# Kernel optimization log

Measured on AMD Instinct MI355X. Metric: run time of the kernel, lower is better.

## Reference

```python
import jax, jax.numpy as jnp
import numpy as np

RING_WORLD_SIZE = 4  # number of ring steps / KV sequence chunks


def _ring_flash_attention(q, k, v, ring_size):
    # q,k,v: [B, S, H, D]; non-causal full attention computed blockwise over
    # KV chunks (one per ring step) with numerically-stable online LSE merge,
    # mirroring _compact_ring_fwd + update_out_and_lse.
    B, S, H, D = q.shape
    scale = D ** (-0.5)
    chunk = S // ring_size
    out = None  # [B, S, H, D] accumulated in fp32
    lse = None  # [B, H, S] running log-sum-exp
    for step in range(ring_size):
        k_blk = jax.lax.dynamic_slice_in_dim(k, step * chunk, chunk, axis=1)
        v_blk = jax.lax.dynamic_slice_in_dim(v, step * chunk, chunk, axis=1)
        # scores: [B, H, Sq, Sk_blk]
        scores = jnp.einsum('bqhd,bkhd->bhqk', q, k_blk) * scale
        block_lse = jax.scipy.special.logsumexp(scores, axis=-1)  # [B,H,Sq]
        probs = jnp.exp(scores - block_lse[..., None])
        block_out = jnp.einsum('bhqk,bkhd->bqhd', probs, v_blk)
        if out is None:
            out, lse = block_out, block_lse
        else:
            new_lse = jnp.logaddexp(lse, block_lse)
            w_old = jnp.exp(lse - new_lse)       # [B,H,Sq]
            w_new = jnp.exp(block_lse - new_lse)
            # broadcast weights to [B,Sq,H,1]
            out = (jnp.transpose(w_old, (0, 2, 1))[..., None] * out
                   + jnp.transpose(w_new, (0, 2, 1))[..., None] * block_out)
            lse = new_lse
    return out.astype(q.dtype)


def setup_inputs() -> dict:
    key = jax.random.key(0)
    kq, kk, kv = jax.random.split(key, 3)
    shape = (1, 4096, 16, 128)
    return {
        'query': jax.random.normal(kq, shape, dtype=jnp.float32),
        'key': jax.random.normal(kk, shape, dtype=jnp.float32),
        'value': jax.random.normal(kv, shape, dtype=jnp.float32),
    }


def reference(query, key, value):
    # Ulysses all-to-all is identity on a single logical device; the ring loop
    # with lossless (error-feedback) KV compression reduces to blockwise
    # attention with online softmax merging.
    return _ring_flash_attention(query, key, value, RING_WORLD_SIZE)
```

## Files before the change

kernel.cpp:

```cpp
#include <hip/hip_runtime.h>
#include <hip/hip_bf16.h>

#define S_LEN 4096
#define NH    16
#define DD    128
#define HD    2048
#define QB    64
#define KB    64
#define NT    (S_LEN/KB)

typedef __bf16 bf16_t;
typedef bf16_t bf16x8 __attribute__((ext_vector_type(8)));
typedef float  f32x4  __attribute__((ext_vector_type(4)));

static __device__ __forceinline__ bf16x8 pack8(float4 a, float4 b, float s) {
  bf16x8 v;
  v[0]=(bf16_t)(a.x*s); v[1]=(bf16_t)(a.y*s); v[2]=(bf16_t)(a.z*s); v[3]=(bf16_t)(a.w*s);
  v[4]=(bf16_t)(b.x*s); v[5]=(bf16_t)(b.y*s); v[6]=(bf16_t)(b.z*s); v[7]=(bf16_t)(b.w*s);
  return v;
}

__global__ __launch_bounds__(256) void prep_k(const float* __restrict__ Kg,
                                              bf16_t* __restrict__ Kp) {
  const int kt = blockIdx.x, h = blockIdx.y, tid = threadIdx.x;
  __shared__ bf16_t tile[KB][DD + 8];
  #pragma unroll
  for (int it = 0; it < 8; ++it) {
    int lin4 = it*256 + tid;
    int r  = lin4 >> 5;
    int dc = (lin4 & 31) * 4;
    float4 a = *(const float4*)(Kg + (size_t)(kt*KB + r)*HD + h*DD + dc);
    tile[r][dc+0]=(bf16_t)a.x; tile[r][dc+1]=(bf16_t)a.y;
    tile[r][dc+2]=(bf16_t)a.z; tile[r][dc+3]=(bf16_t)a.w;
  }
  __syncthreads();
  bf16_t* out = Kp + (size_t)(h*NT + kt)*8192;
  #pragma unroll
  for (int it = 0; it < 4; ++it) {
    int cid = it*256 + tid;
    int f = cid >> 6, l = cid & 63;
    int b = f >> 2, c = f & 3;
    int row = b*16 + (l & 15);
    int d0  = c*32 + (l >> 4)*8;
    bf16x8 v = *(const bf16x8*)(&tile[row][d0]);
    *(bf16x8*)(out + (size_t)cid*8) = v;
  }
}

__global__ __launch_bounds__(256) void prep_v(const float* __restrict__ Vg,
                                              bf16_t* __restrict__ Vp) {
  const int kt = blockIdx.x, h = blockIdx.y, tid = threadIdx.x;
  __shared__ bf16_t tile[KB][DD + 8];
  #pragma unroll
  for (int it = 0; it < 8; ++it) {
    int lin4 = it*256 + tid;
    int r  = lin4 >> 5;
    int dc = (lin4 & 31) * 4;
    float4 a = *(const float4*)(Vg + (size_t)(kt*KB + r)*HD + h*DD + dc);
    tile[r][dc+0]=(bf16_t)a.x; tile[r][dc+1]=(bf16_t)a.y;
    tile[r][dc+2]=(bf16_t)a.z; tile[r][dc+3]=(bf16_t)a.w;
  }
  __syncthreads();
  bf16_t* out = Vp + (size_t)(h*NT + kt)*8192;
  #pragma unroll
  for (int it = 0; it < 4; ++it) {
    int cid = it*256 + tid;
    int f = cid >> 6, l = cid & 63;
    int ks = f >> 3, db = f & 7;
    int d  = db*16 + (l & 15);
    int c0 = ks*32 + (l >> 4)*8;
    bf16x8 v;
    #pragma unroll
    for (int m = 0; m < 8; ++m) {
      int c = c0 + m;
      int k = 32*(c>>5) + 16*((c>>2)&1) + 4*((c>>3)&3) + (c&3);
      v[m] = tile[k][d];
    }
    *(bf16x8*)(out + (size_t)cid*8) = v;
  }
}

__global__ __launch_bounds__(128, 2) void attn_fwd(const float* __restrict__ Qg,
                                                   const bf16_t* __restrict__ Kp,
                                                   const bf16_t* __restrict__ Vp,
                                                   float* __restrict__ Og) {
  const int phys = blockIdx.x;
  const int logical = (phys & 7) * 128 + (phys >> 3);
  const int h  = logical >> 6;
  const int qt = logical & 63;
  const int tid  = threadIdx.x;
  const int wid  = tid >> 6;
  const int lane = tid & 63;
  const int l16  = lane & 15;
  const int lg   = lane >> 4;
  const int lo16 = lane * 16;

  const float qs = 0.08838834764831845f * 1.4426950408889634f;
  bf16x8 qf[2][4];
  #pragma unroll
  for (int g = 0; g < 2; ++g) {
    const int qrow = qt*QB + wid*32 + g*16 + l16;
    const float* qp = Qg + (size_t)qrow*HD + h*DD + lg*8;
    #pragma unroll
    for (int c = 0; c < 4; ++c) {
      float4 a = *(const float4*)(qp + c*32);
      float4 b = *(const float4*)(qp + c*32 + 4);
      qf[g][c] = pack8(a, b, qs);
    }
  }
  bf16x8 onesf;
  #pragma unroll
  for (int j = 0; j < 8; ++j) onesf[j] = (bf16_t)1.0f;

  const char* KpH = (const char*)(Kp + (size_t)h*NT*8192) + lo16;
  const char* VpH = (const char*)(Vp + (size_t)h*NT*8192) + lo16;

  bf16x8 kreg[16];
  #pragma unroll
  for (int f = 0; f < 16; ++f) kreg[f] = *(const bf16x8*)(KpH + (f << 10));

  f32x4 acc[2][8];
  f32x4 acc_l[2];
  #pragma unroll
  for (int g = 0; g < 2; ++g) {
    #pragma unroll
    for (int i = 0; i < 8; ++i) acc[g][i] = (f32x4){0.f,0.f,0.f,0.f};
    acc_l[g] = (f32x4){0.f,0.f,0.f,0.f};
  }
  float m_run[2] = {-__builtin_inff(), -__builtin_inff()};

  for (int kt = 0; kt < NT; ++kt) {
    f32x4 sc[2][4];
    #pragma unroll
    for (int g = 0; g < 2; ++g)
      #pragma unroll
      for (int b = 0; b < 4; ++b) sc[g][b] = (f32x4){0.f,0.f,0.f,0.f};
    __builtin_amdgcn_s_setprio(1);
    #pragma unroll
    for (int b = 0; b < 4; ++b) {
      #pragma unroll
      for (int c = 0; c < 4; ++c) {
        bf16x8 kb = kreg[b*4 + c];
        sc[0][b] = __builtin_amdgcn_mfma_f32_16x16x32_bf16(kb, qf[0][c], sc[0][b], 0, 0, 0);
        sc[1][b] = __builtin_amdgcn_mfma_f32_16x16x32_bf16(kb, qf[1][c], sc[1][b], 0, 0, 0);
      }
    }
    __builtin_amdgcn_s_setprio(0);

    const char* vt = VpH + (size_t)kt*16384;
    bf16x8 va0[8];
    #pragma unroll
    for (int f = 0; f < 8; ++f) va0[f] = *(const bf16x8*)(vt + (f << 10));

    if (kt + 1 < NT) {
      const char* kg = KpH + (size_t)(kt + 1)*16384;
      #pragma unroll
      for (int f = 0; f < 16; ++f) kreg[f] = *(const bf16x8*)(kg + (f << 10));
    }

    bf16x8 pp[2][2];
    #pragma unroll
    for (int g = 0; g < 2; ++g) {
      float pmax;
      {
        float a0 = fmaxf(fmaxf(sc[g][0][0], sc[g][0][1]), sc[g][0][2]);
        float a1 = fmaxf(fmaxf(sc[g][0][3], sc[g][1][0]), sc[g][1][1]);
        float a2 = fmaxf(fmaxf(sc[g][1][2], sc[g][1][3]), sc[g][2][0]);
        float a3 = fmaxf(fmaxf(sc[g][2][1], sc[g][2][2]), sc[g][2][3]);
        float a4 = fmaxf(fmaxf(sc[g][3][0], sc[g][3][1]), sc[g][3][2]);
        float b0 = fmaxf(fmaxf(a0, a1), a2);
        float b1 = fmaxf(fmaxf(a3, a4), sc[g][3][3]);
        pmax = fmaxf(b0, b1);
        pmax = fmaxf(pmax, __shfl_xor(pmax, 16));
        pmax = fmaxf(pmax, __shfl_xor(pmax, 32));
      }
      if (!__all(pmax - m_run[g] <= 8.0f)) {
        float mnew  = fmaxf(m_run[g], pmax);
        float alpha = exp2f(m_run[g] - mnew);
        m_run[g] = mnew;
        #pragma unroll
        for (int i = 0; i < 8; ++i) {
          #pragma unroll
          for (int r = 0; r < 4; ++r) acc[g][i][r] *= alpha;
        }
        #pragma unroll
        for (int r = 0; r < 4; ++r) acc_l[g][r] *= alpha;
      }
      #pragma unroll
      for (int b = 0; b < 4; ++b) {
        #pragma unroll
        for (int r = 0; r < 4; ++r) {
          float p = exp2f(sc[g][b][r] - m_run[g]);
          pp[g][b >> 1][(b & 1)*4 + r] = (bf16_t)p;
        }
      }
    }

    bf16x8 va1[8];
    #pragma unroll
    for (int f = 0; f < 8; ++f) va1[f] = *(const bf16x8*)(vt + ((8 + f) << 10));

    __builtin_amdgcn_s_setprio(1);
    acc_l[0] = __builtin_amdgcn_mfma_f32_16x16x32_bf16(onesf, pp[0][0], acc_l[0], 0, 0, 0);
    acc_l[1] = __builtin_amdgcn_mfma_f32_16x16x32_bf16(onesf, pp[1][0], acc_l[1], 0, 0, 0);
    #pragma unroll
    for (int db = 0; db < 8; ++db) {
      acc[0][db] = __builtin_amdgcn_mfma_f32_16x16x32_bf16(va0[db], pp[0][0], acc[0][db], 0, 0, 0);
      acc[1][db] = __builtin_amdgcn_mfma_f32_16x16x32_bf16(va0[db], pp[1][0], acc[1][db], 0, 0, 0);
    }
    acc_l[0] = __builtin_amdgcn_mfma_f32_16x16x32_bf16(onesf, pp[0][1], acc_l[0], 0, 0, 0);
    acc_l[1] = __builtin_amdgcn_mfma_f32_16x16x32_bf16(onesf, pp[1][1], acc_l[1], 0, 0, 0);
    #pragma unroll
    for (int db = 0; db < 8; ++db) {
      acc[0][db] = __builtin_amdgcn_mfma_f32_16x16x32_bf16(va1[db], pp[0][1], acc[0][db], 0, 0, 0);
      acc[1][db] = __builtin_amdgcn_mfma_f32_16x16x32_bf16(va1[db], pp[1][1], acc[1][db], 0, 0, 0);
    }
    __builtin_amdgcn_s_setprio(0);
  }

  #pragma unroll
  for (int g = 0; g < 2; ++g) {
    const int qrow = qt*QB + wid*32 + g*16 + l16;
    const float inv = 1.0f / acc_l[g][0];
    float* op = Og + (size_t)qrow*HD + h*DD + lg*4;
    #pragma unroll
    for (int db = 0; db < 8; ++db) {
      float4 o;
      o.x = acc[g][db][0]*inv; o.y = acc[g][db][1]*inv;
      o.z = acc[g][db][2]*inv; o.w = acc[g][db][3]*inv;
      *(float4*)(op + db*16) = o;
    }
  }
}

extern "C" void kernel_launch(void* const* d_in, const int* in_sizes, int n_in,
                              void* d_out, int out_size, void* d_ws, size_t ws_size,
                              hipStream_t stream) {
  const float* Q = (const float*)d_in[0];
  const float* K = (const float*)d_in[1];
  const float* V = (const float*)d_in[2];
  float* O = (float*)d_out;
  bf16_t* Kp = (bf16_t*)d_ws;
  bf16_t* Vp = Kp + (size_t)NH*S_LEN*DD;
  prep_k<<<dim3(NT, NH), 256, 0, stream>>>(K, Kp);
  prep_v<<<dim3(NT, NH), 256, 0, stream>>>(V, Vp);
  attn_fwd<<<dim3(1024), 128, 0, stream>>>(Q, Kp, Vp, O);
}
```

Baseline: 200.5 us.

## Split KV range across two blocks per query tile and merge partials

Each query tile's KV sweep is split into two halves handled by separate blocks, doubling the grid from 1024 to 2048 blocks. Each block writes unnormalized partial outputs plus its row sum and running max to workspace. A new merge kernel then combines the two partials with log-sum-exp weights. The aim is to raise occupancy and latency hiding on a grid that was too small for the device. In exchange it adds fp32 partial-output write and read traffic and an extra launch, and it needs a larger workspace.

```diff
diff --git a/kernel.cpp b/kernel.cpp
--- a/kernel.cpp
+++ b/kernel.cpp
@@ -8,6 +8,7 @@
 #define QB    64
 #define KB    64
 #define NT    (S_LEN/KB)
+#define SHN   (S_LEN*NH)
 
 typedef __bf16 bf16_t;
 typedef bf16_t bf16x8 __attribute__((ext_vector_type(8)));
@@ -83,17 +84,22 @@
 __global__ __launch_bounds__(128, 2) void attn_fwd(const float* __restrict__ Qg,
                                                    const bf16_t* __restrict__ Kp,
                                                    const bf16_t* __restrict__ Vp,
-                                                   float* __restrict__ Og) {
+                                                   float* __restrict__ A0,
+                                                   float* __restrict__ A1,
+                                                   float* __restrict__ lmW) {
   const int phys = blockIdx.x;
-  const int logical = (phys & 7) * 128 + (phys >> 3);
-  const int h  = logical >> 6;
-  const int qt = logical & 63;
+  const int logical = (phys & 7) * 256 + (phys >> 3);
+  const int h   = logical >> 7;
+  const int rem = logical & 127;
+  const int qt  = rem >> 1;
+  const int p   = rem & 1;
   const int tid  = threadIdx.x;
   const int wid  = tid >> 6;
   const int lane = tid & 63;
   const int l16  = lane & 15;
   const int lg   = lane >> 4;
   const int lo16 = lane * 16;
+  const int kt0 = p * (NT/2), kt1 = kt0 + (NT/2);
 
   const float qs = 0.08838834764831845f * 1.4426950408889634f;
   bf16x8 qf[2][4];
@@ -116,8 +122,11 @@
   const char* VpH = (const char*)(Vp + (size_t)h*NT*8192) + lo16;
 
   bf16x8 kreg[16];
-  #pragma unroll
-  for (int f = 0; f < 16; ++f) kreg[f] = *(const bf16x8*)(KpH + (f << 10));
+  {
+    const char* kg = KpH + (size_t)kt0*16384;
+    #pragma unroll
+    for (int f = 0; f < 16; ++f) kreg[f] = *(const bf16x8*)(kg + (f << 10));
+  }
 
   f32x4 acc[2][8];
   f32x4 acc_l[2];
@@ -129,7 +138,7 @@
   }
   float m_run[2] = {-__builtin_inff(), -__builtin_inff()};
 
-  for (int kt = 0; kt < NT; ++kt) {
+  for (int kt = kt0; kt < kt1; ++kt) {
     f32x4 sc[2][4];
     #pragma unroll
     for (int g = 0; g < 2; ++g)
@@ -152,7 +161,7 @@
     #pragma unroll
     for (int f = 0; f < 8; ++f) va0[f] = *(const bf16x8*)(vt + (f << 10));
 
-    if (kt + 1 < NT) {
+    if (kt + 1 < kt1) {
       const char* kg = KpH + (size_t)(kt + 1)*16384;
       #pragma unroll
       for (int f = 0; f < 16; ++f) kreg[f] = *(const bf16x8*)(kg + (f << 10));
@@ -190,8 +199,8 @@
       for (int b = 0; b < 4; ++b) {
         #pragma unroll
         for (int r = 0; r < 4; ++r) {
-          float p = exp2f(sc[g][b][r] - m_run[g]);
-          pp[g][b >> 1][(b & 1)*4 + r] = (bf16_t)p;
+          float pv = exp2f(sc[g][b][r] - m_run[g]);
+          pp[g][b >> 1][(b & 1)*4 + r] = (bf16_t)pv;
         }
       }
     }
@@ -218,19 +227,47 @@
     __builtin_amdgcn_s_setprio(0);
   }
 
+  float* Ap = p ? A1 : A0;
   #pragma unroll
   for (int g = 0; g < 2; ++g) {
     const int qrow = qt*QB + wid*32 + g*16 + l16;
-    const float inv = 1.0f / acc_l[g][0];
-    float* op = Og + (size_t)qrow*HD + h*DD + lg*4;
+    float* op = Ap + (size_t)qrow*HD + h*DD + lg*4;
     #pragma unroll
     for (int db = 0; db < 8; ++db) {
       float4 o;
-      o.x = acc[g][db][0]*inv; o.y = acc[g][db][1]*inv;
-      o.z = acc[g][db][2]*inv; o.w = acc[g][db][3]*inv;
+      o.x = acc[g][db][0]; o.y = acc[g][db][1];
+      o.z = acc[g][db][2]; o.w = acc[g][db][3];
       *(float4*)(op + db*16) = o;
     }
-  }
+    if (lg == 0) {
+      size_t row = (size_t)h*S_LEN + qrow;
+      lmW[(size_t)p*131072 + row]         = acc_l[g][0];
+      lmW[(size_t)p*131072 + 65536 + row] = m_run[g];
+    }
+  }
+}
+
+__global__ __launch_bounds__(256) void merge2(const float* __restrict__ A1,
+                                              const float* __restrict__ lmW,
+                                              float* __restrict__ O) {
+  size_t idx = (size_t)blockIdx.x*256 + threadIdx.x;
+  size_t sh = idx >> 5;
+  int hh = (int)(sh & 15);
+  int ss = (int)(sh >> 4);
+  size_t row = (size_t)hh*S_LEN + ss;
+  float l0 = lmW[row],          m0 = lmW[65536 + row];
+  float l1 = lmW[131072 + row], m1 = lmW[196608 + row];
+  float m  = fmaxf(m0, m1);
+  float w0 = exp2f(m0 - m), w1 = exp2f(m1 - m);
+  float inv = 1.0f / (l0*w0 + l1*w1);
+  float4 a0 = *(const float4*)(O  + idx*4);
+  float4 a1 = *(const float4*)(A1 + idx*4);
+  float4 o;
+  o.x = (a0.x*w0 + a1.x*w1)*inv;
+  o.y = (a0.y*w0 + a1.y*w1)*inv;
+  o.z = (a0.z*w0 + a1.z*w1)*inv;
+  o.w = (a0.w*w0 + a1.w*w1)*inv;
+  *(float4*)(O + idx*4) = o;
 }
 
 extern "C" void kernel_launch(void* const* d_in, const int* in_sizes, int n_in,
@@ -241,8 +278,11 @@
   const float* V = (const float*)d_in[2];
   float* O = (float*)d_out;
   bf16_t* Kp = (bf16_t*)d_ws;
-  bf16_t* Vp = Kp + (size_t)NH*S_LEN*DD;
+  bf16_t* Vp = Kp + (size_t)8388608;
+  float*  A1 = (float*)(Vp + (size_t)8388608);
+  float*  lm = A1 + (size_t)8388608;
   prep_k<<<dim3(NT, NH), 256, 0, stream>>>(K, Kp);
   prep_v<<<dim3(NT, NH), 256, 0, stream>>>(V, Vp);
-  attn_fwd<<<dim3(1024), 128, 0, stream>>>(Q, Kp, Vp, O);
-}
+  attn_fwd<<<dim3(2048), 128, 0, stream>>>(Q, Kp, Vp, O, A1, lm);
+  merge2<<<dim3(8192), 256, 0, stream>>>(A1, lm, O);
+}
```

New measurement: 231.5 us. 15.5% more time.
